# Kernel optimization log

Measured on AMD Instinct MI355X. Metric: run time of the kernel, lower is better.

The kernel has to match this reference:

```python
import jax, jax.numpy as jnp
import numpy as np

N, IN_DIM, MLPW, HID, NCLS = 2048, 1024, 16, 256, 4


def setup_inputs() -> dict:
    key = jax.random.key(0)
    ks = jax.random.split(key, 12)
    f32 = jnp.float32
    return {
        "x": jax.random.normal(ks[0], (N, IN_DIM), f32),
        "adj": jax.random.uniform(ks[1], (N, N), f32),
        "xdeg": jax.random.uniform(ks[2], (N, N), f32),
        "ydeg": jax.random.uniform(ks[3], (N, N), f32),
        # edge MLP([3, mlp_width, 2])
        "Wm1": jax.random.normal(ks[4], (3, MLPW), f32) * (1.0 / np.sqrt(3.0)),
        "bm1": jnp.zeros((MLPW,), f32),
        "Wm2": jax.random.normal(ks[5], (MLPW, 2), f32) * (1.0 / np.sqrt(MLPW)),
        "bm2": jnp.zeros((2,), f32),
        # GCN / dense layers (stored as [in, out]; torch Linear applies x @ W.T)
        "Wg1": jax.random.normal(ks[6], (IN_DIM, HID), f32) * (1.0 / np.sqrt(IN_DIM)),
        "Wl2": jax.random.normal(ks[7], (HID, 64), f32) * (1.0 / np.sqrt(HID)),
        "bl2": jnp.zeros((64,), f32),
        "Wg2": jax.random.normal(ks[8], (64, NCLS), f32) * (1.0 / 8.0),
    }


def reference(x, adj, xdeg, ydeg, Wm1, bm1, Wm2, bm2, Wg1, Wl2, bl2, Wg2):
    n = adj.shape[0]
    # Edge-feature MLP mask. The torch code gathers nonzero entries, runs the
    # MLP, scatters back into a zero buffer, then multiplies by adj. Computing
    # the mask densely is mathematically identical because adj * mask is zero
    # wherever adj is zero.
    feats = jnp.stack([adj, xdeg, ydeg], axis=-1)          # [N, N, 3]
    h = jax.nn.relu(feats @ Wm1 + bm1)                     # [N, N, MLPW]
    mask = jax.nn.softmax(h @ Wm2 + bm2, axis=-1)[..., 1]  # [N, N]
    A = adj * mask + jnp.eye(n, dtype=adj.dtype)
    # Symmetric-ish normalization: D_row^{-1/2} A D_col^{-1/2}
    # (the torch diag-matmul chain reduces to this row/col scaling).
    rowsum = jnp.sum(A, axis=1)
    colsum = jnp.sum(A, axis=0)
    dr = jnp.where(rowsum > 0, jax.lax.rsqrt(jnp.where(rowsum > 0, rowsum, 1.0)), 0.0)
    dc = jnp.where(colsum > 0, jax.lax.rsqrt(jnp.where(colsum > 0, colsum, 1.0)), 0.0)
    A = dr[:, None] * A * dc[None, :]
    # GCN layer 1 (dropout = identity in eval mode)
    hid = (A @ (x @ Wg1)) @ Wl2 + bl2                      # [N, 64]
    # GCN layer 2
    out = A @ (hid @ Wg2)                                  # [N, n_classes]
    return out, hid
```

## Files before the change

### kernel.cpp

```cpp
#include <hip/hip_runtime.h>

#define NN 2048
#define MLPW 16

typedef __attribute__((ext_vector_type(8))) short short8v;
typedef __attribute__((ext_vector_type(16))) float float16v;
typedef __attribute__((ext_vector_type(4))) unsigned short ushort4v;
typedef __attribute__((ext_vector_type(8))) unsigned short ushort8v;

__device__ __forceinline__ unsigned short f2b(float f) {
  unsigned int u = __float_as_uint(f);
  unsigned int r = (u + 0x7fffu + ((u >> 16) & 1u)) >> 16;
  return (unsigned short)r;
}
__device__ __forceinline__ float b2f(unsigned short u) {
  return __uint_as_float(((unsigned int)u) << 16);
}

__global__ void __launch_bounds__(256) edge_kernel(
    const float* __restrict__ adj, const float* __restrict__ xdeg,
    const float* __restrict__ ydeg,
    const float* __restrict__ Wm1, const float* __restrict__ bm1,
    const float* __restrict__ Wm2, const float* __restrict__ bm2,
    const float* __restrict__ x, const float* __restrict__ Wg1,
    unsigned short* __restrict__ Abf, float* __restrict__ dr,
    unsigned short* __restrict__ xb, unsigned short* __restrict__ Wg1T) {
  const int tid = threadIdx.x;
  const int b = blockIdx.x;
  if (b >= 3072) {
    const int bo = b - 3072;
    const int n = bo * 2 + (tid >> 7);
    const int k0 = (tid & 127) * 8;
    ushort8v o;
#pragma unroll
    for (int e = 0; e < 8; e++) o[e] = f2b(Wg1[(size_t)(k0 + e) * 256 + n]);
    *(ushort8v*)&Wg1T[(size_t)n * 1024 + k0] = o;
    return;
  }
  if (b >= 2048) {
    const size_t idx = (size_t)(b - 2048) * 2048 + (size_t)tid * 8;
    const float4 u = *(const float4*)&x[idx], v = *(const float4*)&x[idx + 4];
    ushort8v o = {f2b(u.x), f2b(u.y), f2b(u.z), f2b(u.w),
                  f2b(v.x), f2b(v.y), f2b(v.z), f2b(v.w)};
    *(ushort8v*)&xb[idx] = o;
    return;
  }
  __shared__ float w1[48], b1[16], w2[32], b2s[2];
  __shared__ float wsum[4];
  if (tid < 48) w1[tid] = Wm1[tid];
  if (tid < 16) b1[tid] = bm1[tid];
  if (tid < 32) w2[tid] = Wm2[tid];
  if (tid < 2) b2s[tid] = bm2[tid];
  __syncthreads();
  const int i = b;
  const float4* adj4 = (const float4*)(adj + (size_t)i * NN);
  const float4* xd4 = (const float4*)(xdeg + (size_t)i * NN);
  const float4* yd4 = (const float4*)(ydeg + (size_t)i * NN);
  ushort4v* A4 = (ushort4v*)(Abf + (size_t)i * NN);
  float rsum = 0.f;
  for (int j4 = tid; j4 < NN / 4; j4 += 256) {
    float4 av = adj4[j4], xv = xd4[j4], yv = yd4[j4];
    float aa[4] = {av.x, av.y, av.z, av.w};
    float xx[4] = {xv.x, xv.y, xv.z, xv.w};
    float yy[4] = {yv.x, yv.y, yv.z, yv.w};
    ushort4v oo;
#pragma unroll
    for (int e = 0; e < 4; e++) {
      float l0 = b2s[0], l1 = b2s[1];
#pragma unroll
      for (int k = 0; k < MLPW; k++) {
        float h = fmaf(aa[e], w1[k], fmaf(xx[e], w1[16 + k], fmaf(yy[e], w1[32 + k], b1[k])));
        h = fmaxf(h, 0.f);
        l0 = fmaf(h, w2[2 * k], l0);
        l1 = fmaf(h, w2[2 * k + 1], l1);
      }
      float mask = 1.f / (1.f + __expf(l0 - l1));
      float v = aa[e] * mask;
      int j = j4 * 4 + e;
      if (j == i) v += 1.f;
      oo[e] = f2b(v);
      rsum += v;
    }
    A4[j4] = oo;
  }
#pragma unroll
  for (int off = 32; off > 0; off >>= 1) rsum += __shfl_down(rsum, off);
  if ((tid & 63) == 0) wsum[tid >> 6] = rsum;
  __syncthreads();
  if (tid == 0) {
    float t = wsum[0] + wsum[1] + wsum[2] + wsum[3];
    dr[i] = t > 0.f ? rsqrtf(t) : 0.f;
  }
}

__global__ void __launch_bounds__(256) gemm_splitk_kernel(
    const unsigned short* __restrict__ A, const unsigned short* __restrict__ B,
    float* __restrict__ P, int M, int N, int K, int Kc) {
  constexpr int SW = 136;
  __shared__ unsigned short As[64 * SW];
  __shared__ unsigned short Bs[128 * SW];
  const int tid = threadIdx.x;
  const int lane = tid & 63, wave = tid >> 6;
  const int l31 = lane & 31, half = lane >> 5;
  const int mh = wave & 1, nh = wave >> 1;
  const int row0 = blockIdx.y * 64, col0 = blockIdx.x * 128;
  const int kbeg = blockIdx.z * Kc;

  float16v acc0, acc1;
#pragma unroll
  for (int r = 0; r < 16; r++) { acc0[r] = 0.f; acc1[r] = 0.f; }

  for (int k0 = 0; k0 < Kc; k0 += 128) {
#pragma unroll
    for (int i = 0; i < 4; i++) {
      const int id = tid + i * 256;
      const int r = id >> 4, c = id & 15;
      *(ushort8v*)&As[r * SW + c * 8] =
          *(const ushort8v*)&A[(size_t)(row0 + r) * K + kbeg + k0 + c * 8];
    }
#pragma unroll
    for (int i = 0; i < 8; i++) {
      const int id = tid + i * 256;
      const int r = id >> 4, c = id & 15;
      *(ushort8v*)&Bs[r * SW + c * 8] =
          *(const ushort8v*)&B[(size_t)(col0 + r) * K + kbeg + k0 + c * 8];
    }
    __syncthreads();
#pragma unroll
    for (int ks = 0; ks < 8; ks++) {
      short8v a = *(const short8v*)&As[(mh * 32 + l31) * SW + ks * 16 + half * 8];
      short8v b0 = *(const short8v*)&Bs[(nh * 64 + l31) * SW + ks * 16 + half * 8];
      short8v b1 = *(const short8v*)&Bs[(nh * 64 + 32 + l31) * SW + ks * 16 + half * 8];
      acc0 = __builtin_amdgcn_mfma_f32_32x32x16_bf16(a, b0, acc0, 0, 0, 0);
      acc1 = __builtin_amdgcn_mfma_f32_32x32x16_bf16(a, b1, acc1, 0, 0, 0);
    }
    __syncthreads();
  }
  float* Pb = P + ((size_t)blockIdx.z * M + row0 + mh * 32) * N + col0 + nh * 64 + l31;
#pragma unroll
  for (int reg = 0; reg < 16; reg++) {
    const int m = (reg & 3) + 8 * (reg >> 2) + 4 * half;
    Pb[(size_t)m * N] = acc0[reg];
    Pb[(size_t)m * N + 32] = acc1[reg];
  }
}

__global__ void __launch_bounds__(256) dcxwt_kernel(
    const unsigned short* __restrict__ Abf, const float* __restrict__ P1,
    float* __restrict__ dc, unsigned short* __restrict__ XWT) {
  __shared__ float part[64][32];
  __shared__ float dcs[32];
  const int tid = threadIdx.x;
  const int c0 = blockIdx.x * 32;
  {
    const int cA = (tid & 3) * 8, rgA = tid >> 2;
    float sa[8] = {0, 0, 0, 0, 0, 0, 0, 0};
    const unsigned short* ap = Abf + (size_t)rgA * NN + c0 + cA;
#pragma unroll 4
    for (int k = 0; k < 32; k++) {
      ushort8v u = *(const ushort8v*)ap;
#pragma unroll
      for (int e = 0; e < 8; e++) sa[e] += b2f(u[e]);
      ap += (size_t)64 * NN;
    }
#pragma unroll
    for (int e = 0; e < 8; e++) part[rgA][cA + e] = sa[e];
  }
  __syncthreads();
  if (tid < 32) {
    float d = 0.f;
#pragma unroll
    for (int rg = 0; rg < 64; rg++) d += part[rg][tid];
    d = d > 0.f ? rsqrtf(d) : 0.f;
    dcs[tid] = d;
    dc[c0 + tid] = d;
  }
  __syncthreads();
  const int rB = tid >> 3, cq = (tid & 7) * 4;
  float acc[8][4];
#pragma unroll
  for (int p = 0; p < 8; p++)
#pragma unroll
    for (int e = 0; e < 4; e++) acc[p][e] = 0.f;
#pragma unroll
  for (int sk = 0; sk < 8; sk++) {
#pragma unroll
    for (int p = 0; p < 8; p++) {
      const float* pp = P1 + ((size_t)sk * 256 + rB + p * 32) * NN + c0 + cq;
      float4 v = *(const float4*)pp;
      acc[p][0] += v.x; acc[p][1] += v.y; acc[p][2] += v.z; acc[p][3] += v.w;
    }
  }
  const float4 dv = *(const float4*)&dcs[cq];
#pragma unroll
  for (int p = 0; p < 8; p++) {
    ushort4v o = {f2b(acc[p][0] * dv.x), f2b(acc[p][1] * dv.y),
                  f2b(acc[p][2] * dv.z), f2b(acc[p][3] * dv.w)};
    *(ushort4v*)&XWT[(size_t)(rB + p * 32) * NN + c0 + cq] = o;
  }
}

__global__ void __launch_bounds__(256) tail_kernel(
    const float* __restrict__ P2, const float* __restrict__ dr,
    const float* __restrict__ dc, const float* __restrict__ Wl2,
    const float* __restrict__ bl2, const float* __restrict__ Wg2,
    float* __restrict__ hid, float* __restrict__ HW) {
  __shared__ float T1s[8][256];
  __shared__ float hidS[8][68];
  const int m0 = blockIdx.x * 8;
  const int tid = threadIdx.x;
#pragma unroll
  for (int i = 0; i < 8; i++) {
    const int idx = tid + i * 256;
    const int mi = idx >> 8, n = idx & 255;
    float s = 0.f;
#pragma unroll
    for (int sk = 0; sk < 8; sk++)
      s += P2[((size_t)sk * 2048 + m0 + mi) * 256 + n];
    T1s[mi][n] = s * dr[m0 + mi];
  }
  __syncthreads();
  const int j = tid & 63, mg = tid >> 6;
  float h0 = bl2[j], h1 = h0;
#pragma unroll 8
  for (int n = 0; n < 256; n++) {
    float w = Wl2[(size_t)n * 64 + j];
    h0 = fmaf(T1s[mg * 2 + 0][n], w, h0);
    h1 = fmaf(T1s[mg * 2 + 1][n], w, h1);
  }
  hid[(size_t)(m0 + mg * 2 + 0) * 64 + j] = h0;
  hid[(size_t)(m0 + mg * 2 + 1) * 64 + j] = h1;
  hidS[mg * 2 + 0][j] = h0;
  hidS[mg * 2 + 1][j] = h1;
  __syncthreads();
  if (tid < 32) {
    const int r = tid >> 2, c = tid & 3;
    float s = 0.f;
#pragma unroll
    for (int jj = 0; jj < 64; jj++) s = fmaf(hidS[r][jj], Wg2[jj * 4 + c], s);
    HW[(size_t)(m0 + r) * 4 + c] = s * dc[m0 + r];
  }
}

__global__ void __launch_bounds__(256) out_kernel(
    const unsigned short* __restrict__ Abf, const float* __restrict__ HW,
    const float* __restrict__ dr, float* __restrict__ outp) {
  const int i = blockIdx.x, tid = threadIdx.x;
  const ushort8v a8 = ((const ushort8v*)(Abf + (size_t)i * NN))[tid];
  const float4* hw4 = (const float4*)HW;
  const int j0 = tid * 8;
  float ax = 0.f, ay = 0.f, az = 0.f, aw = 0.f;
#pragma unroll
  for (int e = 0; e < 8; e++) {
    float a = b2f(a8[e]);
    float4 h = hw4[j0 + e];
    ax = fmaf(a, h.x, ax);
    ay = fmaf(a, h.y, ay);
    az = fmaf(a, h.z, az);
    aw = fmaf(a, h.w, aw);
  }
#pragma unroll
  for (int off = 32; off > 0; off >>= 1) {
    ax += __shfl_down(ax, off);
    ay += __shfl_down(ay, off);
    az += __shfl_down(az, off);
    aw += __shfl_down(aw, off);
  }
  __shared__ float wsum[4][4];
  const int w = tid >> 6;
  if ((tid & 63) == 0) {
    wsum[w][0] = ax; wsum[w][1] = ay; wsum[w][2] = az; wsum[w][3] = aw;
  }
  __syncthreads();
  if (tid < 4)
    outp[(size_t)i * 4 + tid] =
        dr[i] * (wsum[0][tid] + wsum[1][tid] + wsum[2][tid] + wsum[3][tid]);
}

extern "C" void kernel_launch(void* const* d_in, const int* in_sizes, int n_in,
                              void* d_out, int out_size, void* d_ws, size_t ws_size,
                              hipStream_t stream) {
  const float* x    = (const float*)d_in[0];
  const float* adj  = (const float*)d_in[1];
  const float* xdeg = (const float*)d_in[2];
  const float* ydeg = (const float*)d_in[3];
  const float* Wm1  = (const float*)d_in[4];
  const float* bm1  = (const float*)d_in[5];
  const float* Wm2  = (const float*)d_in[6];
  const float* bm2  = (const float*)d_in[7];
  const float* Wg1  = (const float*)d_in[8];
  const float* Wl2  = (const float*)d_in[9];
  const float* bl2  = (const float*)d_in[10];
  const float* Wg2  = (const float*)d_in[11];

  char* ws = (char*)d_ws;
  unsigned short* Abf  = (unsigned short*)(ws);
  unsigned short* xb   = (unsigned short*)(ws + 8388608);
  unsigned short* Wg1T = (unsigned short*)(ws + 12582912);
  float* P1   = (float*)(ws + 13107200);
  float* P2   = (float*)(ws + 29884416);
  unsigned short* XWT = (unsigned short*)(ws + 46661632);
  float* dr   = (float*)(ws + 47710208);
  float* dc   = (float*)(ws + 47718400);
  float* HW   = (float*)(ws + 47726592);

  float* outp = (float*)d_out;
  float* hid  = (float*)d_out + 2048 * 4;

  edge_kernel<<<3200, 256, 0, stream>>>(adj, xdeg, ydeg, Wm1, bm1, Wm2, bm2,
                                        x, Wg1, Abf, dr, xb, Wg1T);
  gemm_splitk_kernel<<<dim3(2048 / 128, 256 / 64, 8), 256, 0, stream>>>(
      Wg1T, xb, P1, 256, 2048, 1024, 128);
  dcxwt_kernel<<<64, 256, 0, stream>>>(Abf, P1, dc, XWT);
  gemm_splitk_kernel<<<dim3(256 / 128, 2048 / 64, 8), 256, 0, stream>>>(
      Abf, XWT, P2, 2048, 256, 2048, 256);
  tail_kernel<<<2048 / 8, 256, 0, stream>>>(P2, dr, dc, Wl2, bl2, Wg2, hid, HW);
  out_kernel<<<NN, 256, 0, stream>>>(Abf, HW, dr, outp);
}
```

Baseline: 169.3 us.

## Replace split-K X·Wg1 GEMM with full-K GEMM fusing column scaling and bf16 output

The first GEMM (Wg1ᵀ·xᵀ) no longer uses 8-way split-K with fp32 partials written to a 16 MB buffer and reduced in a separate kernel. A dedicated 64x64-tile GEMM now runs the full K=1024 loop, multiplies by the precomputed column normaliser dc and writes bf16 XWT directly, and a small dc_kernel computes dc beforehand. This removes the partial-sum write and readback traffic, but the new GEMM has only 128 blocks, each with a long serial K loop, so it may use the GPU's compute units poorly.

```diff
diff --git a/kernel.cpp b/kernel.cpp
--- a/kernel.cpp
+++ b/kernel.cpp
@@ -93,6 +93,77 @@
   }
 }
 
+__global__ void __launch_bounds__(256) dc_kernel(
+    const unsigned short* __restrict__ Abf, float* __restrict__ dc) {
+  __shared__ float part[64][32];
+  const int tid = threadIdx.x;
+  const int c0 = blockIdx.x * 32;
+  const int cA = (tid & 3) * 8, rgA = tid >> 2;
+  float sa[8] = {0, 0, 0, 0, 0, 0, 0, 0};
+  const unsigned short* ap = Abf + (size_t)rgA * NN + c0 + cA;
+#pragma unroll 4
+  for (int k = 0; k < 32; k++) {
+    ushort8v u = *(const ushort8v*)ap;
+#pragma unroll
+    for (int e = 0; e < 8; e++) sa[e] += b2f(u[e]);
+    ap += (size_t)64 * NN;
+  }
+#pragma unroll
+  for (int e = 0; e < 8; e++) part[rgA][cA + e] = sa[e];
+  __syncthreads();
+  if (tid < 32) {
+    float d = 0.f;
+#pragma unroll
+    for (int rg = 0; rg < 64; rg++) d += part[rg][tid];
+    dc[c0 + tid] = d > 0.f ? rsqrtf(d) : 0.f;
+  }
+}
+
+__global__ void __launch_bounds__(256) gemm1_kernel(
+    const unsigned short* __restrict__ A, const unsigned short* __restrict__ B,
+    const float* __restrict__ dc, unsigned short* __restrict__ XWT) {
+  constexpr int SW = 136;
+  __shared__ unsigned short As[64 * SW];
+  __shared__ unsigned short Bs[64 * SW];
+  const int tid = threadIdx.x;
+  const int lane = tid & 63, wave = tid >> 6;
+  const int l31 = lane & 31, half = lane >> 5;
+  const int mh = wave & 1, nh = wave >> 1;
+  const int row0 = blockIdx.y * 64, col0 = blockIdx.x * 64;
+
+  float16v acc;
+#pragma unroll
+  for (int r = 0; r < 16; r++) acc[r] = 0.f;
+
+  for (int k0 = 0; k0 < 1024; k0 += 128) {
+#pragma unroll
+    for (int i = 0; i < 4; i++) {
+      const int id = tid + i * 256;
+      const int r = id >> 4, c = id & 15;
+      *(ushort8v*)&As[r * SW + c * 8] =
+          *(const ushort8v*)&A[(size_t)(row0 + r) * 1024 + k0 + c * 8];
+      *(ushort8v*)&Bs[r * SW + c * 8] =
+          *(const ushort8v*)&B[(size_t)(col0 + r) * 1024 + k0 + c * 8];
+    }
+    __syncthreads();
+#pragma unroll
+    for (int ks = 0; ks < 8; ks++) {
+      short8v a = *(const short8v*)&As[(mh * 32 + l31) * SW + ks * 16 + half * 8];
+      short8v b = *(const short8v*)&Bs[(nh * 32 + l31) * SW + ks * 16 + half * 8];
+      acc = __builtin_amdgcn_mfma_f32_32x32x16_bf16(a, b, acc, 0, 0, 0);
+    }
+    __syncthreads();
+  }
+  const int n = col0 + nh * 32 + l31;
+  const float dv = dc[n];
+  unsigned short* Xb = XWT + (size_t)(row0 + mh * 32) * NN + n;
+#pragma unroll
+  for (int reg = 0; reg < 16; reg++) {
+    const int m = (reg & 3) + 8 * (reg >> 2) + 4 * half;
+    Xb[(size_t)m * NN] = f2b(acc[reg] * dv);
+  }
+}
+
 __global__ void __launch_bounds__(256) gemm_splitk_kernel(
     const unsigned short* __restrict__ A, const unsigned short* __restrict__ B,
     float* __restrict__ P, int M, int N, int K, int Kc) {
@@ -142,61 +213,6 @@
     const int m = (reg & 3) + 8 * (reg >> 2) + 4 * half;
     Pb[(size_t)m * N] = acc0[reg];
     Pb[(size_t)m * N + 32] = acc1[reg];
-  }
-}
-
-__global__ void __launch_bounds__(256) dcxwt_kernel(
-    const unsigned short* __restrict__ Abf, const float* __restrict__ P1,
-    float* __restrict__ dc, unsigned short* __restrict__ XWT) {
-  __shared__ float part[64][32];
-  __shared__ float dcs[32];
-  const int tid = threadIdx.x;
-  const int c0 = blockIdx.x * 32;
-  {
-    const int cA = (tid & 3) * 8, rgA = tid >> 2;
-    float sa[8] = {0, 0, 0, 0, 0, 0, 0, 0};
-    const unsigned short* ap = Abf + (size_t)rgA * NN + c0 + cA;
-#pragma unroll 4
-    for (int k = 0; k < 32; k++) {
-      ushort8v u = *(const ushort8v*)ap;
-#pragma unroll
-      for (int e = 0; e < 8; e++) sa[e] += b2f(u[e]);
-      ap += (size_t)64 * NN;
-    }
-#pragma unroll
-    for (int e = 0; e < 8; e++) part[rgA][cA + e] = sa[e];
-  }
-  __syncthreads();
-  if (tid < 32) {
-    float d = 0.f;
-#pragma unroll
-    for (int rg = 0; rg < 64; rg++) d += part[rg][tid];
-    d = d > 0.f ? rsqrtf(d) : 0.f;
-    dcs[tid] = d;
-    dc[c0 + tid] = d;
-  }
-  __syncthreads();
-  const int rB = tid >> 3, cq = (tid & 7) * 4;
-  float acc[8][4];
-#pragma unroll
-  for (int p = 0; p < 8; p++)
-#pragma unroll
-    for (int e = 0; e < 4; e++) acc[p][e] = 0.f;
-#pragma unroll
-  for (int sk = 0; sk < 8; sk++) {
-#pragma unroll
-    for (int p = 0; p < 8; p++) {
-      const float* pp = P1 + ((size_t)sk * 256 + rB + p * 32) * NN + c0 + cq;
-      float4 v = *(const float4*)pp;
-      acc[p][0] += v.x; acc[p][1] += v.y; acc[p][2] += v.z; acc[p][3] += v.w;
-    }
-  }
-  const float4 dv = *(const float4*)&dcs[cq];
-#pragma unroll
-  for (int p = 0; p < 8; p++) {
-    ushort4v o = {f2b(acc[p][0] * dv.x), f2b(acc[p][1] * dv.y),
-                  f2b(acc[p][2] * dv.z), f2b(acc[p][3] * dv.w)};
-    *(ushort4v*)&XWT[(size_t)(rB + p * 32) * NN + c0 + cq] = o;
   }
 }
 
@@ -297,21 +313,19 @@
   unsigned short* Abf  = (unsigned short*)(ws);
   unsigned short* xb   = (unsigned short*)(ws + 8388608);
   unsigned short* Wg1T = (unsigned short*)(ws + 12582912);
-  float* P1   = (float*)(ws + 13107200);
-  float* P2   = (float*)(ws + 29884416);
-  unsigned short* XWT = (unsigned short*)(ws + 46661632);
-  float* dr   = (float*)(ws + 47710208);
-  float* dc   = (float*)(ws + 47718400);
-  float* HW   = (float*)(ws + 47726592);
+  unsigned short* XWT  = (unsigned short*)(ws + 13107200);
+  float* P2   = (float*)(ws + 14155776);
+  float* dr   = (float*)(ws + 30932992);
+  float* dc   = (float*)(ws + 30941184);
+  float* HW   = (float*)(ws + 30949376);
 
   float* outp = (float*)d_out;
   float* hid  = (float*)d_out + 2048 * 4;
 
   edge_kernel<<<3200, 256, 0, stream>>>(adj, xdeg, ydeg, Wm1, bm1, Wm2, bm2,
                                         x, Wg1, Abf, dr, xb, Wg1T);
-  gemm_splitk_kernel<<<dim3(2048 / 128, 256 / 64, 8), 256, 0, stream>>>(
-      Wg1T, xb, P1, 256, 2048, 1024, 128);
-  dcxwt_kernel<<<64, 256, 0, stream>>>(Abf, P1, dc, XWT);
+  dc_kernel<<<64, 256, 0, stream>>>(Abf, dc);
+  gemm1_kernel<<<dim3(2048 / 64, 256 / 64), 256, 0, stream>>>(Wg1T, xb, dc, XWT);
   gemm_splitk_kernel<<<dim3(256 / 128, 2048 / 64, 8), 256, 0, stream>>>(
       Abf, XWT, P2, 2048, 256, 2048, 256);
   tail_kernel<<<2048 / 8, 256, 0, stream>>>(P2, dr, dc, Wl2, bl2, Wg2, hid, HW);
```

After: 168.7 us. No clear change (-0.4%).
